# Optimization experiments

Hardware: AMD Instinct MI355X
Metric: run time of the kernel (lower is better)

## Reference

```python
import jax, jax.numpy as jnp
import numpy as np

H = 256           # hidden_size == target_size
GRID = (128, 128)
SAM_W = 2
B, T = 32, 512


def _leaky(x):
    return jax.nn.leaky_relu(x, 0.1)


def _grid_mask(x):
    # mask of valid (non-padding) points, per original grid-id computation
    off = GRID[1] * SAM_W + SAM_W
    g = jnp.clip(x[:, :, 3] * GRID[1] + x[:, :, 2] - off + 1,
                 0, GRID[0] * GRID[1]).astype(jnp.int32)
    return g != 0  # (B, T)


def _lstm(x, Wih, Whh, bih, bhh):
    # x: (T, B, H) -> outputs (T, B, H); 1-layer LSTM, zero init state (torch gate order i,f,g,o)
    h0 = jnp.zeros((x.shape[1], H), x.dtype)

    def step(carry, xt):
        h, c = carry
        g = xt @ Wih.T + h @ Whh.T + (bih + bhh)
        i, f, gg, o = jnp.split(g, 4, axis=-1)
        c = jax.nn.sigmoid(f) * c + jax.nn.sigmoid(i) * jnp.tanh(gg)
        h = jax.nn.sigmoid(o) * jnp.tanh(c)
        return (h, c), h

    _, out = jax.lax.scan(step, (h0, h0), x)
    return out


def _gate(o, W1, b1, W2, b2, W3, b3):
    c = jax.nn.sigmoid(o @ W1.T + b1) * _leaky(o @ W2.T + b2)
    return o + jax.nn.sigmoid(o @ W3.T + b3) * _leaky(c)


def _pair(a, la, b, lb, mask_a, mask_b,
          W_mlp, b_mlp, Wih, Whh, bih, bhh, W1, b1, W2, b2, W3, b3):
    ma = _leaky(a[:, :, :2] @ W_mlp.T + b_mlp)   # (B, Ta, H/2)
    mb = _leaky(b[:, :, :2] @ W_mlp.T + b_mlp)   # (B, Tb, H/2)
    valid = mask_a[:, :, None] & mask_b[:, None, :]              # (B, Ta, Tb)
    scores = jnp.where(valid, jnp.einsum('bth,bsh->bts', ma, mb), -1e9)
    # a attends over b
    pa = jnp.where(valid, jax.nn.softmax(scores, axis=-1), 0.0)
    sum_b = jnp.einsum('bts,bsh->bth', pa, mb)   # == broadcast-mul-sum in original
    out_a = _lstm(jnp.concatenate([ma, ma - sum_b], -1).transpose(1, 0, 2),
                  Wih, Whh, bih, bhh)            # (Ta, B, H)
    fa = _gate(out_a, W1, b1, W2, b2, W3, b3)[la - 1, jnp.arange(la.shape[0])]
    # b attends over a (reuses the same masked scores, transposed)
    pb = jnp.where(valid.transpose(0, 2, 1),
                   jax.nn.softmax(scores.transpose(0, 2, 1), axis=-1), 0.0)
    sum_a = jnp.einsum('but,bth->buh', pb, ma)
    out_b = _lstm(jnp.concatenate([mb, mb - sum_a], -1).transpose(1, 0, 2),
                  Wih, Whh, bih, bhh)            # (Tb, B, H)
    # NOTE: original selects from raw LSTM outputs_b (not gated) for fb_outputs
    fb = out_b[lb - 1, jnp.arange(lb.shape[0])]
    return fa, fb


def _dist(x, y):
    d = x - y + 1e-6  # F.pairwise_distance eps
    return jnp.sqrt(jnp.sum(d * d, axis=-1))


def setup_inputs() -> dict:
    key = jax.random.key(0)
    ks = jax.random.split(key, 16)

    def traj(k1, k2):
        xy = jax.random.normal(k1, (B, T, 2), jnp.float32)
        gc = jax.random.randint(k2, (B, T, 2), 0, GRID[0]).astype(jnp.float32)
        return jnp.concatenate([xy, gc], -1)  # (B, T, 4): lon,lat,gridx,gridy

    inp = {
        'anchor': traj(ks[0], ks[1]),
        'trajs': traj(ks[2], ks[3]),
        'negative': traj(ks[4], ks[5]),
        'anchor_len': jax.random.randint(ks[6], (B,), 1, T + 1),
        'trajs_len': jax.random.randint(ks[7], (B,), 1, T + 1),
        'negative_len': jax.random.randint(ks[8], (B,), 1, T + 1),
    }
    s = 1.0 / np.sqrt(H)
    inp['W_mlp'] = jax.random.normal(ks[9], (H // 2, 2), jnp.float32) * 0.5
    inp['b_mlp'] = jnp.zeros((H // 2,), jnp.float32)
    inp['Wih'] = jax.random.normal(ks[10], (4 * H, H), jnp.float32) * s
    inp['Whh'] = jax.random.normal(ks[11], (4 * H, H), jnp.float32) * s
    inp['bih'] = jnp.zeros((4 * H,), jnp.float32)
    inp['bhh'] = jnp.zeros((4 * H,), jnp.float32)
    for i, n in enumerate(['1', '2', '3']):
        inp['W' + n] = jax.random.normal(ks[12 + i], (H, H), jnp.float32) * s
        inp['b' + n] = jnp.zeros((H,), jnp.float32)
    return inp


def reference(anchor, trajs, negative, anchor_len, trajs_len, negative_len,
              W_mlp, b_mlp, Wih, Whh, bih, bhh, W1, b1, W2, b2, W3, b3):
    p = (W_mlp, b_mlp, Wih, Whh, bih, bhh, W1, b1, W2, b2, W3, b3)
    m_a = _grid_mask(anchor)
    m_t = _grid_mask(trajs)
    m_n = _grid_mask(negative)
    fa1, fb1 = _pair(anchor, anchor_len, trajs, trajs_len, m_a, m_t, *p)
    trajs_loss = jnp.exp(_dist(fa1, fb1))
    fa2, fb2 = _pair(anchor, anchor_len, negative, negative_len, m_a, m_n, *p)
    negative_loss = jnp.exp(_dist(fa2, fb2))
    return trajs_loss, negative_loss
```

## Files before the change

### kernel.cpp

```cpp
#include <hip/hip_runtime.h>

constexpr int BB = 32;
constexpr int TT = 512;
constexpr size_t MSZ = (size_t)BB * TT * 128;
constexpr size_t M_OFF = 0;
constexpr size_t MASK_OFF = 3 * MSZ;
constexpr size_t SUM_OFF = MASK_OFF + (size_t)3 * BB * TT;
constexpr size_t M16_OFF = SUM_OFF + 4 * MSZ;
constexpr size_t MT16_OFF = M16_OFF + 3 * MSZ / 2;
constexpr size_t WHH_OFF = MT16_OFF + 3 * MSZ / 2;
constexpr size_t WIH_OFF = WHH_OFF + (size_t)256 * 1024;
constexpr size_t BIAS_OFF = WIH_OFF + (size_t)256 * 1024;
constexpr size_t W5_OFF = BIAS_OFF + 1024;
constexpr size_t FSEL_OFF = W5_OFF + 131072;
constexpr size_t STATE_OFF = FSEL_OFF + (size_t)128 * 256;
constexpr size_t XGBUF_OFF = STATE_OFF + 65536;

typedef _Float16 h2v __attribute__((ext_vector_type(2)));
typedef _Float16 half8 __attribute__((ext_vector_type(8)));
typedef float f32x4 __attribute__((ext_vector_type(4)));

__device__ __forceinline__ float sigm(float x) {
  return __builtin_amdgcn_rcpf(1.f + __builtin_amdgcn_exp2f(-1.44269504f * x));
}
__device__ __forceinline__ float tanhfast(float x) {
  float e = __builtin_amdgcn_exp2f(2.88539008f * x);
  return 1.f - 2.f * __builtin_amdgcn_rcpf(e + 1.f);
}
__device__ __forceinline__ float leaky(float x) { return x >= 0.f ? x : 0.1f * x; }

__device__ __forceinline__ unsigned int pack2h(float a, float b) {
  h2v h;
  h.x = (_Float16)a;
  h.y = (_Float16)b;
  return __builtin_bit_cast(unsigned int, h);
}

__device__ __forceinline__ float fdot2u(unsigned int a, unsigned int b, float c) {
#if __has_builtin(__builtin_amdgcn_fdot2)
  return __builtin_amdgcn_fdot2(__builtin_bit_cast(h2v, a), __builtin_bit_cast(h2v, b), c, false);
#else
  h2v ha = __builtin_bit_cast(h2v, a), hb = __builtin_bit_cast(h2v, b);
  return c + (float)ha.x * (float)hb.x + (float)ha.y * (float)hb.y;
#endif
}

#define GLOAD_LDS16(gp, lp)                                                    \
  __builtin_amdgcn_global_load_lds(                                            \
      (const __attribute__((address_space(1))) void*)(gp),                     \
      (__attribute__((address_space(3))) void*)(lp), 16, 0, 0)

__global__ __launch_bounds__(256) void embed_kernel(
    const float* __restrict__ a, const float* __restrict__ t,
    const float* __restrict__ n, const float* __restrict__ Wm,
    const float* __restrict__ bm, float* __restrict__ ws) {
  int idx = blockIdx.x * 256 + threadIdx.x;
  int h = idx & 127;
  int bt = idx >> 7;
  int traj = bt / (BB * TT);
  int r = bt - traj * (BB * TT);
  const float* src = traj == 0 ? a : (traj == 1 ? t : n);
  float x0 = src[r * 4 + 0], x1 = src[r * 4 + 1];
  float v = x0 * Wm[2 * h] + x1 * Wm[2 * h + 1] + bm[h];
  ws[M_OFF + (size_t)traj * MSZ + (size_t)r * 128 + h] = leaky(v);
}

__global__ __launch_bounds__(256) void mask_kernel(
    const float* __restrict__ a, const float* __restrict__ t,
    const float* __restrict__ n, float* __restrict__ ws) {
  int idx = blockIdx.x * 256 + threadIdx.x;
  int traj = idx / (BB * TT);
  int r = idx - traj * (BB * TT);
  const float* src = traj == 0 ? a : (traj == 1 ? t : n);
  float gx = src[r * 4 + 2], gy = src[r * 4 + 3];
  ((int*)(ws + MASK_OFF))[idx] = (gy * 128.f + gx - 257.f) >= 0.5f ? 1 : 0;
}

__global__ __launch_bounds__(256) void pack16_kernel(float* __restrict__ ws) {
  size_t idx = (size_t)blockIdx.x * 256 + threadIdx.x;
  float v0 = ws[M_OFF + 2 * idx];
  float v1 = ws[M_OFF + 2 * idx + 1];
  ((unsigned int*)ws)[M16_OFF + idx] = pack2h(v0, v1);
}

__global__ __launch_bounds__(256) void packT_kernel(float* __restrict__ ws) {
  __shared__ float L[64][130];
  int tid = threadIdx.x;
  int traj = blockIdx.x >> 5, b = blockIdx.x & 31;
  const float* src = ws + M_OFF + (size_t)traj * MSZ + (size_t)b * TT * 128;
  size_t basedw = ((size_t)traj * MSZ + (size_t)b * TT * 128) >> 1;
  unsigned int* dst = (unsigned int*)ws + MT16_OFF + basedw;
  for (int tt = 0; tt < 8; tt++) {
    int t0 = tt * 64;
    __syncthreads();
#pragma unroll
    for (int i = 0; i < 32; i++) {
      int idx = i * 256 + tid;
      int tl = idx >> 7, d = idx & 127;
      L[tl][d] = src[(size_t)(t0 + tl) * 128 + d];
    }
    __syncthreads();
#pragma unroll
    for (int i = 0; i < 16; i++) {
      int j = i * 256 + tid;
      int d = j >> 5, tp = j & 31;
      dst[(size_t)d * 256 + (t0 >> 1) + tp] = pack2h(L[2 * tp][d], L[2 * tp + 1][d]);
    }
  }
}

__global__ __launch_bounds__(256) void wt_kernel(
    const float* __restrict__ Wih, const float* __restrict__ Whh,
    const float* __restrict__ bih, const float* __restrict__ bhh,
    float* __restrict__ ws) {
  int idx = blockIdx.x * 256 + threadIdx.x;
  if (idx < 262144) {
    int k = idx >> 10;
    int rest = idx & 1023;
    int hid = rest >> 2, g = rest & 3;
    ws[WHH_OFF + idx] = Whh[(g * 256 + hid) * 256 + k];
  } else if (idx < 524288) {
    int j = idx - 262144;
    int k = j >> 10;
    int rest = j & 1023;
    int hid = rest >> 2, g = rest & 3;
    ws[WIH_OFF + j] = Wih[(g * 256 + hid) * 256 + k];
  } else if (idx < 525312) {
    int j = idx - 524288;
    int hid = j >> 2, g = j & 3;
    ws[BIAS_OFF + j] = bih[g * 256 + hid] + bhh[g * 256 + hid];
  } else if (idx < 656384) {
    int j = idx - 525312;
    int u = j & 3;
    int hid = (j >> 2) & 255;
    int g = (j >> 10) & 15;
    int gate = (j >> 14) & 3;
    int kh = j >> 16;
    int k0 = kh * 128 + g * 8 + u * 2;
    const float* row = Whh + (size_t)(gate * 256 + hid) * 256;
    ((unsigned int*)ws)[W5_OFF + j] = pack2h(row[k0], row[k0 + 1]);
  }
}

__global__ __launch_bounds__(256) void attn2_kernel(float* __restrict__ ws) {
  __shared__ _Float16 srcL[32 * 128];
  __shared__ _Float16 dbuf[128 * 128];
  __shared__ float scf[32 * 521];
  __shared__ _Float16 p16[32 * 512];
  __shared__ float rowscale[32];
  __shared__ int mD[512];
  __shared__ int mS[32];

  int tid = threadIdx.x;
  int w = tid >> 6, lane = tid & 63;
  int l15 = lane & 15, l4 = lane >> 4;
  int bid = blockIdx.x;
  int job = bid >> 9;
  int rem = bid & 511;
  int b = rem >> 4, tb = rem & 15;
  int t0 = tb * 32;
  int srcTr = (job == 1) ? 1 : ((job == 3) ? 2 : 0);
  int dstTr = (job == 0) ? 1 : ((job == 2) ? 2 : 0);
  const _Float16* m16 = (const _Float16*)((const unsigned int*)ws + M16_OFF);
  const _Float16* mT16 = (const _Float16*)((const unsigned int*)ws + MT16_OFF);
  const _Float16* srcb = m16 + (size_t)srcTr * MSZ + (size_t)b * TT * 128;
  const _Float16* dstb = m16 + (size_t)dstTr * MSZ + (size_t)b * TT * 128;
  const _Float16* dstbT = mT16 + (size_t)dstTr * MSZ + (size_t)b * TT * 128;
  const int* maskbase = (const int*)(ws + MASK_OFF);
  const int* smask = maskbase + srcTr * BB * TT + b * TT;
  const int* dmask = maskbase + dstTr * BB * TT + b * TT;
  float* out = ws + SUM_OFF + (size_t)job * MSZ + (size_t)b * TT * 128;

#pragma unroll
  for (int i = 0; i < 2; i++) {
    int inst = w * 2 + i;
    int tl = inst * 4 + l4;
    const char* sp = (const char*)(srcb + (size_t)(t0 + tl) * 128) + ((l15 ^ (tl & 7)) << 4);
    GLOAD_LDS16(sp, (char*)srcL + inst * 1024);
  }
  mD[tid] = dmask[tid];
  mD[tid + 256] = dmask[tid + 256];
  if (tid < 32) mS[tid] = smask[t0 + tid];

  for (int sc = 0; sc < 4; sc++) {
    int s0 = sc * 128;
    __syncthreads();
#pragma unroll
    for (int i = 0; i < 8; i++) {
      int inst = w * 8 + i;
      int rl = inst * 4 + l4;
      const char* sp = (const char*)(dstb + (size_t)(s0 + rl) * 128) + ((l15 ^ (rl & 7)) << 4);
      GLOAD_LDS16(sp, (char*)dbuf + inst * 1024);
    }
    __syncthreads();

    f32x4 c[2][2] = {{{0.f, 0.f, 0.f, 0.f}, {0.f, 0.f, 0.f, 0.f}},
                     {{0.f, 0.f, 0.f, 0.f}, {0.f, 0.f, 0.f, 0.f}}};
#pragma unroll
    for (int kk = 0; kk < 4; kk++) {
      int gc = kk * 4 + l4;
      half8 afr[2], bfr[2];
#pragma unroll
      for (int si = 0; si < 2; si++) {
        int srow = (w * 2 + si) * 16 + l15;
        afr[si] = *(const half8*)(dbuf + srow * 128 + ((gc ^ (srow & 7)) << 3));
      }
#pragma unroll
      for (int ti = 0; ti < 2; ti++) {
        int trow = ti * 16 + l15;
        bfr[ti] = *(const half8*)(srcL + trow * 128 + ((gc ^ (trow & 7)) << 3));
      }
#pragma unroll
      for (int si = 0; si < 2; si++)
#pragma unroll
        for (int ti = 0; ti < 2; ti++)
          c[si][ti] = __builtin_amdgcn_mfma_f32_16x16x32_f16(afr[si], bfr[ti], c[si][ti], 0, 0, 0);
    }
#pragma unroll
    for (int si = 0; si < 2; si++)
#pragma unroll
      for (int ti = 0; ti < 2; ti++) {
        int tl = ti * 16 + l15;
#pragma unroll
        for (int r = 0; r < 4; r++) {
          int sg = s0 + (w * 2 + si) * 16 + l4 * 4 + r;
          scf[tl * 521 + sg] = mD[sg] ? c[si][ti][r] : -1e9f;
        }
      }
  }
  __syncthreads();

  {
    int row = tid >> 3, j = tid & 7;
    const float* sr = &scf[row * 521];
    float mx = -3.0e38f;
#pragma unroll 8
    for (int i = 0; i < 64; i++) mx = fmaxf(mx, sr[j + 8 * i]);
    for (int m = 1; m <= 4; m <<= 1) mx = fmaxf(mx, __shfl_xor(mx, m, 64));
    float den = 0.f;
    float* srw = &scf[row * 521];
#pragma unroll 8
    for (int i = 0; i < 64; i++) {
      float p = __builtin_amdgcn_exp2f((srw[j + 8 * i] - mx) * 1.44269504f);
      srw[j + 8 * i] = p;
      den += p;
    }
    for (int m = 1; m <= 4; m <<= 1) den += __shfl_xor(den, m, 64);
    if (j == 0) rowscale[row] = (mS[row] && mx > -5e8f) ? (1.f / den) : 0.f;
  }
  __syncthreads();

#pragma unroll
  for (int i = 0; i < 64; i++) {
    int idx = i * 256 + tid;
    int t = idx >> 9, s = idx & 511;
    int gp = ((s >> 3) ^ (t & 7));
    p16[t * 512 + gp * 8 + (s & 7)] = (_Float16)scf[t * 521 + s];
  }

  f32x4 o[2][2] = {{{0.f, 0.f, 0.f, 0.f}, {0.f, 0.f, 0.f, 0.f}},
                   {{0.f, 0.f, 0.f, 0.f}, {0.f, 0.f, 0.f, 0.f}}};
  for (int sc = 0; sc < 4; sc++) {
    int s0 = sc * 128;
    __syncthreads();
#pragma unroll
    for (int i = 0; i < 8; i++) {
      int inst = w * 8 + i;
      int rd = inst * 4 + l4;
      const char* sp = (const char*)(dstbT + (size_t)rd * 512 + s0) + ((l15 ^ (rd & 7)) << 4);
      GLOAD_LDS16(sp, (char*)dbuf + inst * 1024);
    }
    __syncthreads();
#pragma unroll
    for (int ks = 0; ks < 4; ks++) {
      int gc = ks * 4 + l4;
      half8 afr[2], bfr[2];
#pragma unroll
      for (int ti = 0; ti < 2; ti++) {
        int t = ti * 16 + l15;
        int sg = sc * 16 + gc;
        afr[ti] = *(const half8*)(p16 + t * 512 + ((sg ^ (t & 7)) << 3));
      }
#pragma unroll
      for (int di = 0; di < 2; di++) {
        int d = (w * 2 + di) * 16 + l15;
        bfr[di] = *(const half8*)(dbuf + d * 128 + ((gc ^ (d & 7)) << 3));
      }
#pragma unroll
      for (int ti = 0; ti < 2; ti++)
#pragma unroll
        for (int di = 0; di < 2; di++)
          o[ti][di] = __builtin_amdgcn_mfma_f32_16x16x32_f16(afr[ti], bfr[di], o[ti][di], 0, 0, 0);
    }
  }
#pragma unroll
  for (int ti = 0; ti < 2; ti++)
#pragma unroll
    for (int di = 0; di < 2; di++) {
      int dglob = (w * 2 + di) * 16 + l15;
#pragma unroll
      for (int r = 0; r < 4; r++) {
        int tl = ti * 16 + l4 * 4 + r;
        out[(size_t)(t0 + tl) * 128 + dglob] = o[ti][di][r] * rowscale[tl];
      }
    }
}

__global__ __launch_bounds__(256) void xg_kernel(
    float* __restrict__ ws, int tc0, int CH,
    const int* __restrict__ la, const int* __restrict__ lt, const int* __restrict__ ln) {
  __shared__ float aT[32][68];
  __shared__ float bL[32][256];
  int tid = threadIdx.x;
  int bx = blockIdx.x;
  int tt4 = (CH >> 6) << 2;
  int seq = bx / tt4;
  int rem = bx - seq * tt4;
  int tt = rem >> 2;
  int nc = rem & 3;
  int t0 = tc0 + tt * 64;
  int l = seq >> 5, b = seq & 31;
  const int* lens = (l == 1) ? lt : ((l == 3) ? ln : la);
  if (t0 >= lens[b]) return;
  int srcTr = (l == 1) ? 1 : ((l == 3) ? 2 : 0);
  const float* xrow = ws + M_OFF + (size_t)srcTr * MSZ + (size_t)b * TT * 128;
  const float* srow = ws + SUM_OFF + (size_t)l * MSZ + (size_t)b * TT * 128;

  int r0 = tid >> 5;
  int c0 = (tid & 31) * 4;

  float acc[8][8];
#pragma unroll
  for (int i = 0; i < 8; i++)
#pragma unroll
    for (int j = 0; j < 8; j++) acc[i][j] = 0.f;

  for (int kc = 0; kc < 8; kc++) {
    int kbase = kc * 32;
    __syncthreads();
#pragma unroll
    for (int i = 0; i < 8; i++) {
      int idx = i * 256 + tid;
      int m = idx >> 5, kkv = idx & 31;
      float v;
      if (kbase < 128) {
        v = xrow[(size_t)(t0 + m) * 128 + kbase + kkv];
      } else {
        int k2 = kbase + kkv - 128;
        v = xrow[(size_t)(t0 + m) * 128 + k2] - srow[(size_t)(t0 + m) * 128 + k2];
      }
      aT[kkv][m] = v;
    }
#pragma unroll
    for (int i = 0; i < 32; i++) {
      int idx = i * 256 + tid;
      int kkv = idx >> 8, n = idx & 255;
      bL[kkv][n] = ws[WIH_OFF + (size_t)(kbase + kkv) * 1024 + nc * 256 + n];
    }
    __syncthreads();
#pragma unroll 2
    for (int kkv = 0; kkv < 32; kkv++) {
      float4 a0 = *(const float4*)&aT[kkv][r0 * 8];
      float4 a1 = *(const float4*)&aT[kkv][r0 * 8 + 4];
      float4 b0 = *(const float4*)&bL[kkv][c0];
      float4 b1 = *(const float4*)&bL[kkv][c0 + 128];
      float av[8] = {a0.x, a0.y, a0.z, a0.w, a1.x, a1.y, a1.z, a1.w};
      float bv[8] = {b0.x, b0.y, b0.z, b0.w, b1.x, b1.y, b1.z, b1.w};
#pragma unroll
      for (int i = 0; i < 8; i++)
#pragma unroll
        for (int j = 0; j < 8; j++) acc[i][j] += av[i] * bv[j];
    }
  }

  float4 bias0 = *(const float4*)&ws[BIAS_OFF + nc * 256 + c0];
  float4 bias1 = *(const float4*)&ws[BIAS_OFF + nc * 256 + c0 + 128];
#pragma unroll
  for (int i = 0; i < 8; i++) {
    int tl = t0 - tc0 + r0 * 8 + i;
    float* o = ws + XGBUF_OFF + ((size_t)seq * CH + tl) * 1024 + nc * 256 + c0;
    float4 v0 = {acc[i][0] + bias0.x, acc[i][1] + bias0.y,
                 acc[i][2] + bias0.z, acc[i][3] + bias0.w};
    float4 v1 = {acc[i][4] + bias1.x, acc[i][5] + bias1.y,
                 acc[i][6] + bias1.z, acc[i][7] + bias1.w};
    *(float4*)o = v0;
    *(float4*)(o + 128) = v1;
  }
}

__global__ __launch_bounds__(512, 2) void rec5_kernel(
    float* __restrict__ ws, const int* __restrict__ la,
    const int* __restrict__ lt, const int* __restrict__ ln,
    int t0c, int CH) {
  __shared__ unsigned int o_w[32768];
  __shared__ unsigned int hp[128];
  __shared__ float4 part[256];
  int tid = threadIdx.x;
  int hid = tid & 255;
  int kh = tid >> 8;
  int seq = blockIdx.x;
  int l = seq >> 5, b = seq & 31;
  int mylen = (l == 1) ? lt[b] : ((l == 3) ? ln[b] : la[b]);
  int tend = min(CH, mylen - t0c);
  if (tend <= 0) return;

  const unsigned int* W5 = (const unsigned int*)ws + W5_OFF;

  uint4 wi[16], wf[16], wg[16];
  {
    const unsigned int* base = W5 + (size_t)kh * 65536 + hid * 4;
#pragma unroll
    for (int g = 0; g < 16; g++) {
      wi[g] = *(const uint4*)(base + (0 * 16 + g) * 1024);
      wf[g] = *(const uint4*)(base + (1 * 16 + g) * 1024);
      wg[g] = *(const uint4*)(base + (2 * 16 + g) * 1024);
    }
  }
  {
    int wv = tid >> 6;
    int khw = wv >> 2;
    int hidbase = (wv & 3) * 64;
    const unsigned int* srcb = W5 + (size_t)(khw * 4 + 3) * 16384 + (hidbase + (tid & 63)) * 4;
#pragma unroll
    for (int g = 0; g < 16; g++) {
      GLOAD_LDS16(srcb + g * 1024, &o_w[((khw * 16 + g) * 256 + hidbase) * 4]);
    }
  }

  float c_st = 0.f, hlast = 0.f;
  if (t0c == 0) {
    if (tid < 128) hp[tid] = 0u;
  } else {
    if (tid < 128) {
      float h0 = ws[STATE_OFF + (size_t)seq * 256 + 2 * tid];
      float h1 = ws[STATE_OFF + (size_t)seq * 256 + 2 * tid + 1];
      hp[tid] = pack2h(h0, h1);
    }
    if (kh == 0) {
      hlast = ws[STATE_OFF + (size_t)seq * 256 + hid];
      c_st = ws[STATE_OFF + 32768 + (size_t)seq * 256 + hid];
    }
  }
  const float* xgrow = ws + XGBUF_OFF + ((size_t)seq * CH) * 1024 + hid * 4;
  float* fout = ws + FSEL_OFF + (size_t)seq * 256;
  __syncthreads();

  for (int tl = 0; tl < tend; tl++) {
    float ai = 0.f, af = 0.f, ag = 0.f, ao = 0.f;
    const unsigned int* hb = &hp[kh * 64];
#pragma unroll
    for (int g = 0; g < 16; g++) {
      uint4 h4 = *(const uint4*)(hb + g * 4);
      uint4 o4 = *(const uint4*)&o_w[((kh * 16 + g) * 256 + hid) * 4];
      ai = fdot2u(wi[g].x, h4.x, ai); ai = fdot2u(wi[g].y, h4.y, ai);
      ai = fdot2u(wi[g].z, h4.z, ai); ai = fdot2u(wi[g].w, h4.w, ai);
      af = fdot2u(wf[g].x, h4.x, af); af = fdot2u(wf[g].y, h4.y, af);
      af = fdot2u(wf[g].z, h4.z, af); af = fdot2u(wf[g].w, h4.w, af);
      ag = fdot2u(wg[g].x, h4.x, ag); ag = fdot2u(wg[g].y, h4.y, ag);
      ag = fdot2u(wg[g].z, h4.z, ag); ag = fdot2u(wg[g].w, h4.w, ag);
      ao = fdot2u(o4.x, h4.x, ao); ao = fdot2u(o4.y, h4.y, ao);
      ao = fdot2u(o4.z, h4.z, ao); ao = fdot2u(o4.w, h4.w, ao);
    }
    if (kh == 1) part[hid] = make_float4(ai, af, ag, ao);
    __syncthreads();
    if (kh == 0) {
      float4 p2 = part[hid];
      float4 xv = *(const float4*)(xgrow + (size_t)tl * 1024);
      float gi = ai + p2.x + xv.x;
      float gf = af + p2.y + xv.y;
      float gg = ag + p2.z + xv.z;
      float go_ = ao + p2.w + xv.w;
      c_st = sigm(gf) * c_st + sigm(gi) * tanhfast(gg);
      float h = sigm(go_) * tanhfast(c_st);
      hlast = h;
      ((_Float16*)hp)[hid] = (_Float16)h;
      if (t0c + tl == mylen - 1) fout[hid] = h;
    }
    __syncthreads();
  }
  if (kh == 0) {
    ws[STATE_OFF + (size_t)seq * 256 + hid] = hlast;
    ws[STATE_OFF + 32768 + (size_t)seq * 256 + hid] = c_st;
  }
}

__global__ __launch_bounds__(512, 2) void rec_fb_kernel(
    float* __restrict__ ws, const int* __restrict__ la,
    const int* __restrict__ lt, const int* __restrict__ ln) {
  __shared__ float hL[2][256];
  __shared__ float xL[2][256];
  int tid = threadIdx.x;
  int sl = tid >> 8;
  int hid = tid & 255;
  int seq = blockIdx.x * 2 + sl;
  int l = seq >> 5, b = seq & 31;
  int srcTr = (l == 1) ? 1 : ((l == 3) ? 2 : 0);
  const float* xrow = ws + M_OFF + (size_t)srcTr * MSZ + (size_t)b * TT * 128;
  const float* srow = ws + SUM_OFF + (size_t)l * MSZ + (size_t)b * TT * 128;
  const int* lens = (l == 1) ? lt : ((l == 3) ? ln : la);
  int mylen = lens[b];
  const float* wh = ws + WHH_OFF + (hid << 2);
  const float* wi = ws + WIH_OFF + (hid << 2);
  float4 biasv = *(const float4*)&ws[BIAS_OFF + (hid << 2)];
  float c = 0.f;
  hL[sl][hid] = 0.f;
  xL[sl][hid] = hid < 128 ? xrow[hid] : xrow[hid - 128] - srow[hid - 128];
  __syncthreads();
  float* fout = ws + FSEL_OFF + (size_t)seq * 256;

  for (int t = 0; t < TT; t++) {
    float gi = biasv.x, gf = biasv.y, gg = biasv.z, go = biasv.w;
    {
      const float* hp = &hL[sl][0];
#pragma unroll 4
      for (int k = 0; k < 256; k += 4) {
        float4 hv = *(const float4*)(hp + k);
        const float* w = wh + (size_t)k * 1024;
        float4 w0 = *(const float4*)(w);
        float4 w1 = *(const float4*)(w + 1024);
        float4 w2 = *(const float4*)(w + 2048);
        float4 w3 = *(const float4*)(w + 3072);
        gi += hv.x * w0.x + hv.y * w1.x + hv.z * w2.x + hv.w * w3.x;
        gf += hv.x * w0.y + hv.y * w1.y + hv.z * w2.y + hv.w * w3.y;
        gg += hv.x * w0.z + hv.y * w1.z + hv.z * w2.z + hv.w * w3.z;
        go += hv.x * w0.w + hv.y * w1.w + hv.z * w2.w + hv.w * w3.w;
      }
    }
    {
      const float* xp = &xL[sl][0];
#pragma unroll 4
      for (int k = 0; k < 256; k += 4) {
        float4 xv = *(const float4*)(xp + k);
        const float* w = wi + (size_t)k * 1024;
        float4 w0 = *(const float4*)(w);
        float4 w1 = *(const float4*)(w + 1024);
        float4 w2 = *(const float4*)(w + 2048);
        float4 w3 = *(const float4*)(w + 3072);
        gi += xv.x * w0.x + xv.y * w1.x + xv.z * w2.x + xv.w * w3.x;
        gf += xv.x * w0.y + xv.y * w1.y + xv.z * w2.y + xv.w * w3.y;
        gg += xv.x * w0.z + xv.y * w1.z + xv.z * w2.z + xv.w * w3.z;
        go += xv.x * w0.w + xv.y * w1.w + xv.z * w2.w + xv.w * w3.w;
      }
    }
    float c_new = sigm(gf) * c + sigm(gi) * tanhfast(gg);
    c = c_new;
    float h = sigm(go) * tanhfast(c_new);
    __syncthreads();
    hL[sl][hid] = h;
    if (t + 1 < TT) {
      int tn = t + 1;
      xL[sl][hid] = hid < 128 ? xrow[tn * 128 + hid]
                              : xrow[tn * 128 + hid - 128] - srow[tn * 128 + hid - 128];
    }
    if (t == mylen - 1) fout[hid] = h;
    __syncthreads();
  }
}

__global__ __launch_bounds__(256) void finish_kernel(
    const float* __restrict__ ws, const float* __restrict__ W1,
    const float* __restrict__ b1, const float* __restrict__ W2,
    const float* __restrict__ b2, const float* __restrict__ W3,
    const float* __restrict__ b3, float* __restrict__ out) {
  __shared__ float oL[256];
  __shared__ float wsum[4];
  int tid = threadIdx.x;
  int p = blockIdx.x >> 5, b = blockIdx.x & 31;
  const float* fa = ws + FSEL_OFF + (size_t)((2 * p) * 32 + b) * 256;
  const float* fb = ws + FSEL_OFF + (size_t)((2 * p + 1) * 32 + b) * 256;
  oL[tid] = fa[tid];
  __syncthreads();
  float a1 = b1[tid], a2 = b2[tid], a3 = b3[tid];
  const float* w1r = W1 + tid * 256;
  const float* w2r = W2 + tid * 256;
  const float* w3r = W3 + tid * 256;
  for (int k = 0; k < 256; k++) {
    float ov = oL[k];
    a1 += ov * w1r[k];
    a2 += ov * w2r[k];
    a3 += ov * w3r[k];
  }
  float cg = sigm(a1) * leaky(a2);
  float res = oL[tid] + sigm(a3) * leaky(cg);
  float d = res - fb[tid] + 1e-6f;
  float sq = d * d;
  for (int m = 32; m >= 1; m >>= 1) sq += __shfl_down(sq, m, 64);
  if ((tid & 63) == 0) wsum[tid >> 6] = sq;
  __syncthreads();
  if (tid == 0) {
    float s = wsum[0] + wsum[1] + wsum[2] + wsum[3];
    out[p * BB + b] = expf(sqrtf(s));
  }
}

extern "C" void kernel_launch(void* const* d_in, const int* in_sizes, int n_in,
                              void* d_out, int out_size, void* d_ws, size_t ws_size,
                              hipStream_t stream) {
  const float* anchor = (const float*)d_in[0];
  const float* trajs = (const float*)d_in[1];
  const float* negat = (const float*)d_in[2];
  const int* la = (const int*)d_in[3];
  const int* lt = (const int*)d_in[4];
  const int* ln = (const int*)d_in[5];
  const float* Wm = (const float*)d_in[6];
  const float* bm = (const float*)d_in[7];
  const float* Wih = (const float*)d_in[8];
  const float* Whh = (const float*)d_in[9];
  const float* bih = (const float*)d_in[10];
  const float* bhh = (const float*)d_in[11];
  const float* W1 = (const float*)d_in[12];
  const float* b1 = (const float*)d_in[13];
  const float* W2 = (const float*)d_in[14];
  const float* b2 = (const float*)d_in[15];
  const float* W3 = (const float*)d_in[16];
  const float* b3 = (const float*)d_in[17];
  float* ws = (float*)d_ws;
  float* out = (float*)d_out;

  embed_kernel<<<(3 * BB * TT * 128) / 256, 256, 0, stream>>>(anchor, trajs, negat, Wm, bm, ws);
  mask_kernel<<<(3 * BB * TT) / 256, 256, 0, stream>>>(anchor, trajs, negat, ws);
  pack16_kernel<<<(int)(3 * MSZ / 2 / 256), 256, 0, stream>>>(ws);
  packT_kernel<<<96, 256, 0, stream>>>(ws);
  wt_kernel<<<2564, 256, 0, stream>>>(Wih, Whh, bih, bhh, ws);
  attn2_kernel<<<2048, 256, 0, stream>>>(ws);

  size_t basebytes = XGBUF_OFF * sizeof(float);
  int CH = 0;
  const int cands[4] = {512, 256, 128, 64};
  for (int i = 0; i < 4; i++) {
    size_t need = basebytes + (size_t)cands[i] * 128 * 1024 * sizeof(float);
    if (need <= ws_size) { CH = cands[i]; break; }
  }
  if (CH) {
    int nch = TT / CH;
    int xgrid = 128 * ((CH >> 6) << 2);
    for (int c = 0; c < nch; c++) {
      int tc0 = c * CH;
      xg_kernel<<<xgrid, 256, 0, stream>>>(ws, tc0, CH, la, lt, ln);
      rec5_kernel<<<128, 512, 0, stream>>>(ws, la, lt, ln, tc0, CH);
    }
  } else {
    rec_fb_kernel<<<64, 512, 0, stream>>>(ws, la, lt, ln);
  }
  finish_kernel<<<64, 256, 0, stream>>>(ws, W1, b1, W2, b2, W3, b3, out);
}
```

Before: 1.422 ms.

## Pair K-halves in adjacent lanes, reduce via shuffle, double-buffer hidden state

The recurrent LSTM kernel now puts the two K-halves of each hidden unit in adjacent lanes instead of separate thread halves. Their partial gate sums are combined with a lane shuffle rather than an LDS exchange plus a barrier. The hidden-state LDS buffer is double-buffered, so each timestep needs one barrier instead of two. An empty asm pins the register-resident weights, and the gate nonlinearity now runs with half the lanes masked in every wave, where before it ran in only half the waves.

```diff
diff --git a/kernel.cpp b/kernel.cpp
--- a/kernel.cpp
+++ b/kernel.cpp
@@ -44,6 +44,8 @@
   return c + (float)ha.x * (float)hb.x + (float)ha.y * (float)hb.y;
 #endif
 }
+
+#define PIN4(v) asm volatile("" : "+v"((v).x), "+v"((v).y), "+v"((v).z), "+v"((v).w))
 
 #define GLOAD_LDS16(gp, lp)                                                    \
   __builtin_amdgcn_global_load_lds(                                            \
@@ -388,16 +390,15 @@
   }
 }
 
-__global__ __launch_bounds__(512, 2) void rec5_kernel(
+__global__ __launch_bounds__(512, 2) void rec6_kernel(
     float* __restrict__ ws, const int* __restrict__ la,
     const int* __restrict__ lt, const int* __restrict__ ln,
     int t0c, int CH) {
   __shared__ unsigned int o_w[32768];
-  __shared__ unsigned int hp[128];
-  __shared__ float4 part[256];
+  __shared__ unsigned int hp[2][128];
   int tid = threadIdx.x;
-  int hid = tid & 255;
-  int kh = tid >> 8;
+  int hid = tid >> 1;
+  int kh = tid & 1;
   int seq = blockIdx.x;
   int l = seq >> 5, b = seq & 31;
   int mylen = (l == 1) ? lt[b] : ((l == 3) ? ln[b] : la[b]);
@@ -416,6 +417,13 @@
       wg[g] = *(const uint4*)(base + (2 * 16 + g) * 1024);
     }
   }
+#pragma unroll
+  for (int g = 0; g < 16; g++) {
+    PIN4(wi[g]);
+    PIN4(wf[g]);
+    PIN4(wg[g]);
+  }
+
   {
     int wv = tid >> 6;
     int khw = wv >> 2;
@@ -423,18 +431,18 @@
     const unsigned int* srcb = W5 + (size_t)(khw * 4 + 3) * 16384 + (hidbase + (tid & 63)) * 4;
 #pragma unroll
     for (int g = 0; g < 16; g++) {
-      GLOAD_LDS16(srcb + g * 1024, &o_w[((khw * 16 + g) * 256 + hidbase) * 4]);
+      GLOAD_LDS16(srcb + g * 1024, &o_w[(khw * 16 + g) * 1024 + hidbase * 4]);
     }
   }
 
   float c_st = 0.f, hlast = 0.f;
   if (t0c == 0) {
-    if (tid < 128) hp[tid] = 0u;
+    if (tid < 128) hp[0][tid] = 0u;
   } else {
     if (tid < 128) {
       float h0 = ws[STATE_OFF + (size_t)seq * 256 + 2 * tid];
       float h1 = ws[STATE_OFF + (size_t)seq * 256 + 2 * tid + 1];
-      hp[tid] = pack2h(h0, h1);
+      hp[0][tid] = pack2h(h0, h1);
     }
     if (kh == 0) {
       hlast = ws[STATE_OFF + (size_t)seq * 256 + hid];
@@ -445,13 +453,14 @@
   float* fout = ws + FSEL_OFF + (size_t)seq * 256;
   __syncthreads();
 
+  int pb = 0;
   for (int tl = 0; tl < tend; tl++) {
     float ai = 0.f, af = 0.f, ag = 0.f, ao = 0.f;
-    const unsigned int* hb = &hp[kh * 64];
+    const unsigned int* hb = &hp[pb][kh * 64];
 #pragma unroll
     for (int g = 0; g < 16; g++) {
       uint4 h4 = *(const uint4*)(hb + g * 4);
-      uint4 o4 = *(const uint4*)&o_w[((kh * 16 + g) * 256 + hid) * 4];
+      uint4 o4 = *(const uint4*)&o_w[(kh * 16 + g) * 1024 + hid * 4];
       ai = fdot2u(wi[g].x, h4.x, ai); ai = fdot2u(wi[g].y, h4.y, ai);
       ai = fdot2u(wi[g].z, h4.z, ai); ai = fdot2u(wi[g].w, h4.w, ai);
       af = fdot2u(wf[g].x, h4.x, af); af = fdot2u(wf[g].y, h4.y, af);
@@ -461,22 +470,21 @@
       ao = fdot2u(o4.x, h4.x, ao); ao = fdot2u(o4.y, h4.y, ao);
       ao = fdot2u(o4.z, h4.z, ao); ao = fdot2u(o4.w, h4.w, ao);
     }
-    if (kh == 1) part[hid] = make_float4(ai, af, ag, ao);
-    __syncthreads();
+    ai += __shfl_xor(ai, 1, 64);
+    af += __shfl_xor(af, 1, 64);
+    ag += __shfl_xor(ag, 1, 64);
+    ao += __shfl_xor(ao, 1, 64);
     if (kh == 0) {
-      float4 p2 = part[hid];
       float4 xv = *(const float4*)(xgrow + (size_t)tl * 1024);
-      float gi = ai + p2.x + xv.x;
-      float gf = af + p2.y + xv.y;
-      float gg = ag + p2.z + xv.z;
-      float go_ = ao + p2.w + xv.w;
+      float gi = ai + xv.x, gf = af + xv.y, gg = ag + xv.z, go_ = ao + xv.w;
       c_st = sigm(gf) * c_st + sigm(gi) * tanhfast(gg);
       float h = sigm(go_) * tanhfast(c_st);
       hlast = h;
-      ((_Float16*)hp)[hid] = (_Float16)h;
+      ((_Float16*)hp[pb ^ 1])[hid] = (_Float16)h;
       if (t0c + tl == mylen - 1) fout[hid] = h;
     }
     __syncthreads();
+    pb ^= 1;
   }
   if (kh == 0) {
     ws[STATE_OFF + (size_t)seq * 256 + hid] = hlast;
@@ -637,7 +645,7 @@
     for (int c = 0; c < nch; c++) {
       int tc0 = c * CH;
       xg_kernel<<<xgrid, 256, 0, stream>>>(ws, tc0, CH, la, lt, ln);
-      rec5_kernel<<<128, 512, 0, stream>>>(ws, la, lt, ln, tc0, CH);
+      rec6_kernel<<<128, 512, 0, stream>>>(ws, la, lt, ln, tc0, CH);
     }
   } else {
     rec_fb_kernel<<<64, 512, 0, stream>>>(ws, la, lt, ln);
```

Result: slower. 1.459 ms (+2.6%).
